# Kernel tuning notes

Hardware: AMD Instinct MI355X
Metric: run time of the kernel (lower is better)

Reference implementation:

```python
import jax, jax.numpy as jnp
import numpy as np

N_NODES = 50000


def _gcn_layer(x, src, dst, norm_src, norm_dst, W, b, act):
    # DGL GraphConv with norm='both': D_out^{-1/2} A D_in^{-1/2} X W + b
    h = x * norm_src[:, None]                      # scale by src out-degree
    m = h[src]                                     # gather messages [E, d]
    agg = jax.ops.segment_sum(m, dst, num_segments=N_NODES)  # scatter-add
    agg = agg * norm_dst[:, None]
    out = agg @ W + b
    if act:
        out = jax.nn.relu(out)
    return out


def setup_inputs() -> dict:
    key = jax.random.key(0)
    ks = jax.random.split(key, 10)
    E = 800000
    in_size, hid, out_size = 128, 128, 64
    features = jax.random.normal(ks[0], (N_NODES, in_size), dtype=jnp.float32)
    src = jax.random.randint(ks[1], (E,), 0, N_NODES, dtype=jnp.int32)
    dst = jax.random.randint(ks[2], (E,), 0, N_NODES, dtype=jnp.int32)
    s = 0.05
    W1 = jax.random.normal(ks[3], (in_size, hid), dtype=jnp.float32) * s
    b1 = jnp.zeros((hid,), dtype=jnp.float32)
    W2 = jax.random.normal(ks[4], (hid, hid), dtype=jnp.float32) * s
    b2 = jnp.zeros((hid,), dtype=jnp.float32)
    W3 = jax.random.normal(ks[5], (hid, out_size), dtype=jnp.float32) * s
    b3 = jnp.zeros((out_size,), dtype=jnp.float32)
    return {"features": features, "W1": W1, "b1": b1, "W2": W2, "b2": b2,
            "W3": W3, "b3": b3, "src": src, "dst": dst}


def reference(features, W1, b1, W2, b2, W3, b3, src, dst):
    ones = jnp.ones(src.shape, dtype=features.dtype)
    out_deg = jax.ops.segment_sum(ones, src, num_segments=N_NODES)
    in_deg = jax.ops.segment_sum(ones, dst, num_segments=N_NODES)
    norm_src = jnp.maximum(out_deg, 1.0) ** -0.5   # clamp(min=1) as in DGL
    norm_dst = jnp.maximum(in_deg, 1.0) ** -0.5
    h = _gcn_layer(features, src, dst, norm_src, norm_dst, W1, b1, act=True)
    # dropout is identity in eval mode
    h = _gcn_layer(h, src, dst, norm_src, norm_dst, W2, b2, act=True)
    h = _gcn_layer(h, src, dst, norm_src, norm_dst, W3, b3, act=False)
    return h
```

## Files before the change

kernel.cpp:

```cpp
#include <hip/hip_runtime.h>
#include <math.h>

#define N_NODES 50000
#define K_DIM 128
#define CAP 64
#define CHUNK 25000
#define RH 25000
#define HWORDS 12500

typedef __attribute__((ext_vector_type(8))) short short8_t;
typedef __attribute__((ext_vector_type(4))) float f32x4_t;
typedef __attribute__((ext_vector_type(8))) _Float16 half8_t;

__device__ inline unsigned short f2bf(float x) {
    unsigned u = __float_as_uint(x);
    unsigned r = u + 0x7fffu + ((u >> 16) & 1u);
    return (unsigned short)(r >> 16);
}
__device__ inline float bf2f(unsigned short h) {
    return __uint_as_float(((unsigned)h) << 16);
}


__global__ __launch_bounds__(1024) void hist_kernel(const int* __restrict__ src,
                                                    const int* __restrict__ dst, int E,
                                                    unsigned* __restrict__ pin,
                                                    unsigned* __restrict__ pout) {
    __shared__ unsigned h[HWORDS];
    int b  = blockIdx.x >> 2;
    int io = (blockIdx.x >> 1) & 1;
    int r  = blockIdx.x & 1;
    int tid = threadIdx.x;
    for (int t = tid; t < HWORDS; t += 1024) h[t] = 0;
    __syncthreads();
    const int* keys = io ? src : dst;
    int start = b * CHUNK;
    int end = start + CHUNK; if (end > E) end = E;
    int vlo = r * RH;
    for (int i = start + tid; i < end; i += 1024) {
        int v = keys[i] - vlo;
        if ((unsigned)v < (unsigned)RH)
            atomicAdd(&h[v >> 1], 1u << ((v & 1) * 16));
    }
    __syncthreads();
    unsigned* out = io ? pout : pin;
    for (int t = tid; t < HWORDS; t += 1024)
        out[(size_t)b * (2 * HWORDS) + r * HWORDS + t] = h[t];
}

__global__ void offsets_norm_kernel(const unsigned* __restrict__ pin,
                                    const unsigned* __restrict__ pout,
                                    unsigned short* __restrict__ off16,
                                    int* __restrict__ indeg,
                                    float* __restrict__ nsrc, float* __restrict__ ndst,
                                    int n, int NB) {
    int v = blockIdx.x * blockDim.x + threadIdx.x;
    if (v >= n) return;
    int wi = v >> 1, sh = (v & 1) * 16;
    int od = 0;
    for (int b = 0; b < NB; ++b)
        od += (pout[(size_t)b * (2 * HWORDS) + wi] >> sh) & 0xffff;
    int run = 0;
    for (int b = 0; b < NB; ++b) {
        int c = (pin[(size_t)b * (2 * HWORDS) + wi] >> sh) & 0xffff;
        off16[(size_t)b * n + v] = (unsigned short)(run < CAP ? run : CAP);
        run += c;
    }
    indeg[v] = run < CAP ? run : CAP;
    int odc = od < 1 ? 1 : od;
    int idc = run < 1 ? 1 : run;
    nsrc[v] = 1.0f / sqrtf((float)odc);
    ndst[v] = 1.0f / sqrtf((float)idc);
}

__global__ __launch_bounds__(1024) void scatter_kernel(const int* __restrict__ src,
                                                       const int* __restrict__ dst, int E,
                                                       const unsigned short* __restrict__ off16,
                                                       int* __restrict__ csr, int n) {
    __shared__ unsigned cur[HWORDS];
    int b = blockIdx.x >> 1;
    int r = blockIdx.x & 1;
    int tid = threadIdx.x;
    int vlo = r * RH;
    const unsigned short* offb = off16 + (size_t)b * n + vlo;
    for (int t = tid; t < HWORDS; t += 1024)
        cur[t] = (unsigned)offb[2 * t] | ((unsigned)offb[2 * t + 1] << 16);
    __syncthreads();
    int start = b * CHUNK;
    int end = start + CHUNK; if (end > E) end = E;
    for (int i = start + tid; i < end; i += 1024) {
        int v = dst[i];
        int vr = v - vlo;
        if ((unsigned)vr < (unsigned)RH) {
            int sh = (vr & 1) * 16;
            unsigned old = atomicAdd(&cur[vr >> 1], 1u << sh);
            unsigned p = (old >> sh) & 0xffff;
            if (p < CAP) csr[((size_t)v << 6) + p] = src[i];
        }
    }
}

__global__ void split_w_frag_kernel(const float* __restrict__ W,
                                    unsigned short* __restrict__ WBh,
                                    unsigned short* __restrict__ WBl, int M) {
    int i = blockIdx.x * blockDim.x + threadIdx.x;
    int total = (M / 16) * 4 * 64;
    if (i >= total) return;
    int c    = i >> 8;
    int rem  = i & 255;
    int kc   = rem >> 6;
    int lane = rem & 63;
    int m = lane & 15, q = lane >> 4;
    int n = c * 16 + m;
    #pragma unroll
    for (int j = 0; j < 8; ++j) {
        int k = kc * 32 + q * 8 + j;
        float w = W[(size_t)k * M + n];
        unsigned short hi = f2bf(w);
        unsigned short lo = f2bf(w - bf2f(hi));
        WBh[(size_t)i * 8 + j] = hi;
        WBl[(size_t)i * 8 + j] = lo;
    }
}

template <int M>
__global__ __launch_bounds__(256) void gemm_mfma_kernel(
        const float* __restrict__ X,
        const unsigned short* __restrict__ WBh_,
        const unsigned short* __restrict__ WBl_,
        const float* __restrict__ nsrc, _Float16* __restrict__ Yh, int n) {
    constexpr int LSTR = 136;
    __shared__ short Xhi[64 * LSTR];
    __shared__ short Xlo[64 * LSTR];
    int tid = threadIdx.x;
    int lane = tid & 63, wave = tid >> 6;
    int rowBlock = blockIdx.x * 64;

    #pragma unroll
    for (int l = 0; l < 8; ++l) {
        int idx = (tid + l * 256) * 4;
        int r = idx >> 7;
        int c = idx & 127;
        float4 v = make_float4(0.f, 0.f, 0.f, 0.f);
        int gr = rowBlock + r;
        if (gr < n) v = *(const float4*)&X[(size_t)gr * K_DIM + c];
        unsigned short h0 = f2bf(v.x), h1 = f2bf(v.y), h2 = f2bf(v.z), h3 = f2bf(v.w);
        short4 hs = {(short)h0, (short)h1, (short)h2, (short)h3};
        short4 ls = {(short)f2bf(v.x - bf2f(h0)), (short)f2bf(v.y - bf2f(h1)),
                     (short)f2bf(v.z - bf2f(h2)), (short)f2bf(v.w - bf2f(h3))};
        *(short4*)&Xhi[r * LSTR + c] = hs;
        *(short4*)&Xlo[r * LSTR + c] = ls;
    }
    __syncthreads();

    int m = lane & 15, q = lane >> 4;
    short8_t ah[4], al[4];
    {
        int abase = (wave * 16 + m) * LSTR + q * 8;
        #pragma unroll
        for (int kc = 0; kc < 4; ++kc) {
            ah[kc] = *(const short8_t*)&Xhi[abase + kc * 32];
            al[kc] = *(const short8_t*)&Xlo[abase + kc * 32];
        }
    }
    float ns[4];
    int orow0 = rowBlock + wave * 16 + q * 4;
    #pragma unroll
    for (int r = 0; r < 4; ++r) ns[r] = (orow0 + r < n) ? nsrc[orow0 + r] : 0.f;

    const short8_t* WBh = (const short8_t*)WBh_;
    const short8_t* WBl = (const short8_t*)WBl_;
    constexpr int CT = M / 16;
    #pragma unroll
    for (int c = 0; c < CT; ++c) {
        short8_t bh[4], bl[4];
        #pragma unroll
        for (int kc = 0; kc < 4; ++kc) {
            bh[kc] = WBh[(c * 4 + kc) * 64 + lane];
            bl[kc] = WBl[(c * 4 + kc) * 64 + lane];
        }
        f32x4_t acc = {0.f, 0.f, 0.f, 0.f};
        #pragma unroll
        for (int kc = 0; kc < 4; ++kc) {
            acc = __builtin_amdgcn_mfma_f32_16x16x32_bf16(ah[kc], bh[kc], acc, 0, 0, 0);
            acc = __builtin_amdgcn_mfma_f32_16x16x32_bf16(ah[kc], bl[kc], acc, 0, 0, 0);
            acc = __builtin_amdgcn_mfma_f32_16x16x32_bf16(al[kc], bh[kc], acc, 0, 0, 0);
        }
        int col = c * 16 + m;
        #pragma unroll
        for (int r = 0; r < 4; ++r) {
            int row = orow0 + r;
            if (row < n) Yh[(size_t)row * M + col] = (_Float16)(acc[r] * ns[r]);
        }
    }
}

template <int M, bool RELU>
__global__ __launch_bounds__(256) void agg_kernel(const _Float16* __restrict__ Y,
                                                  const int* __restrict__ indeg,
                                                  const int* __restrict__ csr,
                                                  const float* __restrict__ ndst,
                                                  const float* __restrict__ bias,
                                                  float* __restrict__ Z, int n) {
    constexpr int LPN = M / 8;
    constexpr int NPB = 256 / LPN;
    int v = blockIdx.x * NPB + threadIdx.x / LPN;
    if (v >= n) return;
    int f8 = (threadIdx.x % LPN) * 8;
    int deg = indeg[v];
    const int* __restrict__ row = &csr[(size_t)v * CAP];
    float acc[8] = {};
    for (int i = 0; i < deg; i += 4) {
        int4 ss = *(const int4*)&row[i];
        int s0 = ss.x;
        int s1 = (i + 1 < deg) ? ss.y : N_NODES;
        int s2 = (i + 2 < deg) ? ss.z : N_NODES;
        int s3 = (i + 3 < deg) ? ss.w : N_NODES;
        half8_t a = *(const half8_t*)&Y[(size_t)s0 * M + f8];
        half8_t b = *(const half8_t*)&Y[(size_t)s1 * M + f8];
        half8_t c = *(const half8_t*)&Y[(size_t)s2 * M + f8];
        half8_t d = *(const half8_t*)&Y[(size_t)s3 * M + f8];
        #pragma unroll
        for (int j = 0; j < 8; ++j)
            acc[j] += ((float)a[j] + (float)b[j]) + ((float)c[j] + (float)d[j]);
    }
    float nd = ndst[v];
    float4 bb0 = *(const float4*)&bias[f8];
    float4 bb1 = *(const float4*)&bias[f8 + 4];
    float o[8];
    o[0] = nd * acc[0] + bb0.x; o[1] = nd * acc[1] + bb0.y;
    o[2] = nd * acc[2] + bb0.z; o[3] = nd * acc[3] + bb0.w;
    o[4] = nd * acc[4] + bb1.x; o[5] = nd * acc[5] + bb1.y;
    o[6] = nd * acc[6] + bb1.z; o[7] = nd * acc[7] + bb1.w;
    if (RELU) {
        #pragma unroll
        for (int j = 0; j < 8; ++j) o[j] = fmaxf(o[j], 0.f);
    }
    *(float4*)&Z[(size_t)v * M + f8]     = make_float4(o[0], o[1], o[2], o[3]);
    *(float4*)&Z[(size_t)v * M + f8 + 4] = make_float4(o[4], o[5], o[6], o[7]);
}


extern "C" void kernel_launch(void* const* d_in, const int* in_sizes, int n_in,
                              void* d_out, int out_size, void* d_ws, size_t ws_size,
                              hipStream_t stream) {
    const float* features = (const float*)d_in[0];
    const float* W1 = (const float*)d_in[1];
    const float* b1 = (const float*)d_in[2];
    const float* W2 = (const float*)d_in[3];
    const float* b2 = (const float*)d_in[4];
    const float* W3 = (const float*)d_in[5];
    const float* b3 = (const float*)d_in[6];
    const int* src = (const int*)d_in[7];
    const int* dst = (const int*)d_in[8];
    const int E = in_sizes[7];
    const int N = N_NODES;
    const int NB = (E + CHUNK - 1) / CHUNK;

    char* w = (char*)d_ws;
    auto alloc = [&](size_t bytes) {
        char* p = w;
        w += (bytes + 255) & ~(size_t)255;
        return p;
    };
    _Float16* Yh  = (_Float16*)alloc((size_t)(N + 1) * 128 * 2);
    float* Zbuf   = (float*)alloc((size_t)N * 128 * 4);
    int*   csr    = (int*)alloc((size_t)N * CAP * 4);
    unsigned* pin  = (unsigned*)alloc((size_t)NB * 2 * HWORDS * 4);
    unsigned* pout = (unsigned*)alloc((size_t)NB * 2 * HWORDS * 4);
    unsigned short* off16 = (unsigned short*)alloc((size_t)NB * N * 2);
    int*   indeg  = (int*)alloc((size_t)N * 4);
    float* nsrc   = (float*)alloc((size_t)N * 4);
    float* ndst   = (float*)alloc((size_t)N * 4);
    unsigned short* W1h = (unsigned short*)alloc(128 * 128 * 2);
    unsigned short* W1l = (unsigned short*)alloc(128 * 128 * 2);
    unsigned short* W2h = (unsigned short*)alloc(128 * 128 * 2);
    unsigned short* W2l = (unsigned short*)alloc(128 * 128 * 2);
    unsigned short* W3h = (unsigned short*)alloc(64 * 128 * 2);
    unsigned short* W3l = (unsigned short*)alloc(64 * 128 * 2);

    hipMemsetAsync(Yh + (size_t)N * 128, 0, 128 * 2, stream);

    hist_kernel<<<NB * 4, 1024, 0, stream>>>(src, dst, E, pin, pout);
    offsets_norm_kernel<<<(N + 255) / 256, 256, 0, stream>>>(pin, pout, off16, indeg,
                                                             nsrc, ndst, N, NB);
    scatter_kernel<<<NB * 2, 1024, 0, stream>>>(src, dst, E, off16, csr, N);
    split_w_frag_kernel<<<8, 256, 0, stream>>>(W1, W1h, W1l, 128);
    split_w_frag_kernel<<<8, 256, 0, stream>>>(W2, W2h, W2l, 128);
    split_w_frag_kernel<<<4, 256, 0, stream>>>(W3, W3h, W3l, 64);

    int gblocks = (N + 63) / 64;
    gemm_mfma_kernel<128><<<gblocks, 256, 0, stream>>>(features, W1h, W1l, nsrc, Yh, N);
    agg_kernel<128, true><<<(N + 15) / 16, 256, 0, stream>>>(Yh, indeg, csr, ndst, b1, Zbuf, N);
    gemm_mfma_kernel<128><<<gblocks, 256, 0, stream>>>(Zbuf, W2h, W2l, nsrc, Yh, N);
    agg_kernel<128, true><<<(N + 15) / 16, 256, 0, stream>>>(Yh, indeg, csr, ndst, b2, Zbuf, N);
    hipMemsetAsync(Yh + (size_t)N * 64, 0, 64 * 2, stream);
    gemm_mfma_kernel<64><<<gblocks, 256, 0, stream>>>(Zbuf, W3h, W3l, nsrc, Yh, N);
    agg_kernel<64, false><<<(N + 31) / 32, 256, 0, stream>>>(Yh, indeg, csr, ndst, b3, (float*)d_out, N);
}
```

Before: 263.6 us.

## Fuse aggregation with next-layer GEMM via shared-memory tile and merge weight splits

Adds an agg_gemm kernel that gathers neighbour rows for a 64-node tile, applies norm, bias and ReLU, splits the result into bf16 hi/lo in shared memory, and runs the next layer's MFMA GEMM directly. This removes the fp32 Z buffer round trip through global memory and two kernel launches. The three weight-split launches are merged into one, and the memsets are replaced by a small zero-init kernel that uses separate ping-pong Y buffers. The trade-off is lower occupancy from about 34KB of LDS per block, and gather latency may now sit in front of the GEMM inside each block.

```diff
diff --git a/kernel.cpp b/kernel.cpp
--- a/kernel.cpp
+++ b/kernel.cpp
@@ -19,6 +19,15 @@
 }
 __device__ inline float bf2f(unsigned short h) {
     return __uint_as_float(((unsigned)h) << 16);
+}
+
+__global__ void init_zero_kernel(_Float16* Yx, _Float16* Yy, _Float16* Yz) {
+    int t = threadIdx.x;
+    if (t < 128) {
+        Yx[(size_t)N_NODES * 128 + t] = (_Float16)0.f;
+        Yy[(size_t)N_NODES * 128 + t] = (_Float16)0.f;
+    }
+    if (t < 64) Yz[(size_t)N_NODES * 64 + t] = (_Float16)0.f;
 }
 
 
@@ -100,12 +109,18 @@
     }
 }
 
-__global__ void split_w_frag_kernel(const float* __restrict__ W,
-                                    unsigned short* __restrict__ WBh,
-                                    unsigned short* __restrict__ WBl, int M) {
-    int i = blockIdx.x * blockDim.x + threadIdx.x;
-    int total = (M / 16) * 4 * 64;
-    if (i >= total) return;
+__global__ void split_w_all_kernel(const float* __restrict__ W1,
+                                   const float* __restrict__ W2,
+                                   const float* __restrict__ W3,
+                                   unsigned short* __restrict__ W1h, unsigned short* __restrict__ W1l,
+                                   unsigned short* __restrict__ W2h, unsigned short* __restrict__ W2l,
+                                   unsigned short* __restrict__ W3h, unsigned short* __restrict__ W3l) {
+    int gi = blockIdx.x * blockDim.x + threadIdx.x;
+    const float* W; unsigned short *WBh, *WBl; int M, i;
+    if (gi < 2048)      { W = W1; WBh = W1h; WBl = W1l; M = 128; i = gi; }
+    else if (gi < 4096) { W = W2; WBh = W2h; WBl = W2l; M = 128; i = gi - 2048; }
+    else if (gi < 5120) { W = W3; WBh = W3h; WBl = W3l; M = 64;  i = gi - 4096; }
+    else return;
     int c    = i >> 8;
     int rem  = i & 255;
     int kc   = rem >> 6;
@@ -191,6 +206,107 @@
         for (int r = 0; r < 4; ++r) {
             int row = orow0 + r;
             if (row < n) Yh[(size_t)row * M + col] = (_Float16)(acc[r] * ns[r]);
+        }
+    }
+}
+
+template <int MOUT>
+__global__ __launch_bounds__(256) void agg_gemm_kernel(
+        const _Float16* __restrict__ Yin,
+        const int* __restrict__ indeg, const int* __restrict__ csr,
+        const float* __restrict__ ndst, const float* __restrict__ bias,
+        const unsigned short* __restrict__ WBh_,
+        const unsigned short* __restrict__ WBl_,
+        const float* __restrict__ nsrc, _Float16* __restrict__ Yout, int n) {
+    constexpr int LSTR = 136;
+    __shared__ short Xhi[64 * LSTR];
+    __shared__ short Xlo[64 * LSTR];
+    int tid = threadIdx.x;
+    int lane = tid & 63, wave = tid >> 6;
+    int rowBlock = blockIdx.x * 64;
+
+    int sub = tid >> 4;
+    int f8  = (tid & 15) * 8;
+    #pragma unroll
+    for (int p = 0; p < 4; ++p) {
+        int r = p * 16 + sub;
+        int v = rowBlock + r;
+        float o[8] = {};
+        if (v < n) {
+            int deg = indeg[v];
+            const int* __restrict__ row = &csr[(size_t)v * CAP];
+            float acc[8] = {};
+            for (int i = 0; i < deg; i += 4) {
+                int4 ss = *(const int4*)&row[i];
+                int s0 = ss.x;
+                int s1 = (i + 1 < deg) ? ss.y : N_NODES;
+                int s2 = (i + 2 < deg) ? ss.z : N_NODES;
+                int s3 = (i + 3 < deg) ? ss.w : N_NODES;
+                half8_t a = *(const half8_t*)&Yin[(size_t)s0 * 128 + f8];
+                half8_t b = *(const half8_t*)&Yin[(size_t)s1 * 128 + f8];
+                half8_t c = *(const half8_t*)&Yin[(size_t)s2 * 128 + f8];
+                half8_t d = *(const half8_t*)&Yin[(size_t)s3 * 128 + f8];
+                #pragma unroll
+                for (int j = 0; j < 8; ++j)
+                    acc[j] += ((float)a[j] + (float)b[j]) + ((float)c[j] + (float)d[j]);
+            }
+            float nd = ndst[v];
+            #pragma unroll
+            for (int j = 0; j < 8; ++j)
+                o[j] = fmaxf(nd * acc[j] + bias[f8 + j], 0.f);
+        }
+        short hs[8], ls[8];
+        #pragma unroll
+        for (int j = 0; j < 8; ++j) {
+            unsigned short h = f2bf(o[j]);
+            hs[j] = (short)h;
+            ls[j] = (short)f2bf(o[j] - bf2f(h));
+        }
+        *(short4*)&Xhi[r * LSTR + f8]     = *(short4*)&hs[0];
+        *(short4*)&Xhi[r * LSTR + f8 + 4] = *(short4*)&hs[4];
+        *(short4*)&Xlo[r * LSTR + f8]     = *(short4*)&ls[0];
+        *(short4*)&Xlo[r * LSTR + f8 + 4] = *(short4*)&ls[4];
+    }
+    __syncthreads();
+
+    int m = lane & 15, q = lane >> 4;
+    short8_t ah[4], al[4];
+    {
+        int abase = (wave * 16 + m) * LSTR + q * 8;
+        #pragma unroll
+        for (int kc = 0; kc < 4; ++kc) {
+            ah[kc] = *(const short8_t*)&Xhi[abase + kc * 32];
+            al[kc] = *(const short8_t*)&Xlo[abase + kc * 32];
+        }
+    }
+    float ns[4];
+    int orow0 = rowBlock + wave * 16 + q * 4;
+    #pragma unroll
+    for (int r = 0; r < 4; ++r) ns[r] = (orow0 + r < n) ? nsrc[orow0 + r] : 0.f;
+
+    const short8_t* WBh = (const short8_t*)WBh_;
+    const short8_t* WBl = (const short8_t*)WBl_;
+    constexpr int CT = MOUT / 16;
+    #pragma unroll
+    for (int c = 0; c < CT; ++c) {
+        short8_t bh[4], bl[4];
+        #pragma unroll
+        for (int kc = 0; kc < 4; ++kc) {
+            bh[kc] = WBh[(c * 4 + kc) * 64 + lane];
+            bl[kc] = WBl[(c * 4 + kc) * 64 + lane];
+        }
+        f32x4_t acc = {0.f, 0.f, 0.f, 0.f};
+        #pragma unroll
+        for (int kc = 0; kc < 4; ++kc) {
+            acc = __builtin_amdgcn_mfma_f32_16x16x32_bf16(ah[kc], bh[kc], acc, 0, 0, 0);
+            acc = __builtin_amdgcn_mfma_f32_16x16x32_bf16(ah[kc], bl[kc], acc, 0, 0, 0);
+            acc = __builtin_amdgcn_mfma_f32_16x16x32_bf16(al[kc], bh[kc], acc, 0, 0, 0);
+        }
+        int col = c * 16 + m;
+        #pragma unroll
+        for (int r = 0; r < 4; ++r) {
+            int row = orow0 + r;
+            if (row < n) Yout[(size_t)row * MOUT + col] = (_Float16)(acc[r] * ns[r]);
         }
     }
 }
@@ -263,8 +379,9 @@
         w += (bytes + 255) & ~(size_t)255;
         return p;
     };
-    _Float16* Yh  = (_Float16*)alloc((size_t)(N + 1) * 128 * 2);
-    float* Zbuf   = (float*)alloc((size_t)N * 128 * 4);
+    _Float16* Yx = (_Float16*)alloc((size_t)(N + 1) * 128 * 2);
+    _Float16* Yy = (_Float16*)alloc((size_t)(N + 1) * 128 * 2);
+    _Float16* Yz = (_Float16*)alloc((size_t)(N + 1) * 64 * 2);
     int*   csr    = (int*)alloc((size_t)N * CAP * 4);
     unsigned* pin  = (unsigned*)alloc((size_t)NB * 2 * HWORDS * 4);
     unsigned* pout = (unsigned*)alloc((size_t)NB * 2 * HWORDS * 4);
@@ -279,22 +396,19 @@
     unsigned short* W3h = (unsigned short*)alloc(64 * 128 * 2);
     unsigned short* W3l = (unsigned short*)alloc(64 * 128 * 2);
 
-    hipMemsetAsync(Yh + (size_t)N * 128, 0, 128 * 2, stream);
-
+    init_zero_kernel<<<1, 128, 0, stream>>>(Yx, Yy, Yz);
     hist_kernel<<<NB * 4, 1024, 0, stream>>>(src, dst, E, pin, pout);
     offsets_norm_kernel<<<(N + 255) / 256, 256, 0, stream>>>(pin, pout, off16, indeg,
                                                              nsrc, ndst, N, NB);
     scatter_kernel<<<NB * 2, 1024, 0, stream>>>(src, dst, E, off16, csr, N);
-    split_w_frag_kernel<<<8, 256, 0, stream>>>(W1, W1h, W1l, 128);
-    split_w_frag_kernel<<<8, 256, 0, stream>>>(W2, W2h, W2l, 128);
-    split_w_frag_kernel<<<4, 256, 0, stream>>>(W3, W3h, W3l, 64);
+    split_w_all_kernel<<<20, 256, 0, stream>>>(W1, W2, W3, W1h, W1l, W2h, W2l, W3h, W3l);
 
     int gblocks = (N + 63) / 64;
-    gemm_mfma_kernel<128><<<gblocks, 256, 0, stream>>>(features, W1h, W1l, nsrc, Yh, N);
-    agg_kernel<128, true><<<(N + 15) / 16, 256, 0, stream>>>(Yh, indeg, csr, ndst, b1, Zbuf, N);
-    gemm_mfma_kernel<128><<<gblocks, 256, 0, stream>>>(Zbuf, W2h, W2l, nsrc, Yh, N);
-    agg_kernel<128, true><<<(N + 15) / 16, 256, 0, stream>>>(Yh, indeg, csr, ndst, b2, Zbuf, N);
-    hipMemsetAsync(Yh + (size_t)N * 64, 0, 64 * 2, stream);
-    gemm_mfma_kernel<64><<<gblocks, 256, 0, stream>>>(Zbuf, W3h, W3l, nsrc, Yh, N);
-    agg_kernel<64, false><<<(N + 31) / 32, 256, 0, stream>>>(Yh, indeg, csr, ndst, b3, (float*)d_out, N);
-}
+    gemm_mfma_kernel<128><<<gblocks, 256, 0, stream>>>(features, W1h, W1l, nsrc, Yx, N);
+    agg_gemm_kernel<128><<<gblocks, 256, 0, stream>>>(Yx, indeg, csr, ndst, b1,
+                                                      W2h, W2l, nsrc, Yy, N);
+    agg_gemm_kernel<64><<<gblocks, 256, 0, stream>>>(Yy, indeg, csr, ndst, b2,
+                                                     W3h, W3l, nsrc, Yz, N);
+    agg_kernel<64, false><<<(N + 31) / 32, 256, 0, stream>>>(Yz, indeg, csr, ndst, b3,
+                                                             (float*)d_out, N);
+}
```

New measurement: 244.2 us (median of 2 runs). 1.08x faster.
